# Kernel optimization log

Hardware: AMD Instinct MI355X
Metric: run time of the kernel (lower is better)

Reference implementation:

```python
import jax, jax.numpy as jnp
import numpy as np

B, T, H = 32, 4096, 512


def setup_inputs() -> dict:
    key = jax.random.key(0)
    k1, k2, k3, k4, k5 = jax.random.split(key, 5)
    stdv = 1.0 / np.sqrt(2 * H)
    stdv_v = 1.0 / np.sqrt(H)
    return {
        "hidden": jax.random.normal(k1, (B, H), dtype=jnp.float32),
        "encoder_outputs": jax.random.normal(k2, (T, B, H), dtype=jnp.float32),
        "W_attn": jax.random.uniform(k3, (H, 2 * H), minval=-stdv, maxval=stdv, dtype=jnp.float32),
        "b_attn": jax.random.uniform(k4, (H,), minval=-stdv, maxval=stdv, dtype=jnp.float32),
        "v": jax.random.uniform(k5, (H,), minval=-stdv_v, maxval=stdv_v, dtype=jnp.float32),
    }


def reference(hidden, encoder_outputs, W_attn, b_attn, v):
    # hidden: [B, H]; encoder_outputs: [T, B, H]
    T_ = encoder_outputs.shape[0]
    h = jnp.broadcast_to(hidden[None, :, :], (T_,) + hidden.shape).transpose(1, 0, 2)  # [B,T,H]
    enc = encoder_outputs.transpose(1, 0, 2)  # [B,T,H]
    cat = jnp.concatenate([h, enc], axis=2)  # [B,T,2H]
    # Linear(2H -> H) then legacy F.softmax with implicit dim=0 for 3D input (batch axis)
    energy = jax.nn.softmax(jnp.einsum('btk,hk->bth', cat, W_attn) + b_attn, axis=0)  # [B,T,H]
    # bmm(v[B,1,H], energy^T[B,H,T]) -> [B,1,T] -> squeeze -> [B,T]
    scores = jnp.einsum('h,bth->bt', v, energy)
    return jax.nn.relu(scores)[:, None, :]  # [B,1,T]
```

## Files before the change

kernel.cpp:

```cpp
#include <hip/hip_runtime.h>
#include <hip/hip_bf16.h>

#define B_ 32
#define T_ 4096
#define H_ 512
#define TILE_T 4
#define M_TILE 128
#define BK 64
#define KSTEPS 8
#define NTHREADS 512

typedef __attribute__((ext_vector_type(8))) short short8;
typedef __attribute__((ext_vector_type(8))) __bf16 bf16x8;
typedef __attribute__((ext_vector_type(4))) float f32x4;

__device__ __forceinline__ short f2bf(float f) {
    unsigned u = __builtin_bit_cast(unsigned, f);
    u = (u + 0x7fffu + ((u >> 16) & 1u)) >> 16;
    return (short)u;
}

__global__ void prep_w2(const float* __restrict__ W, short* __restrict__ w2p) {
    int idx = blockIdx.x * 256 + threadIdx.x;
    int kp = idx & 63;
    int h  = (idx >> 6) & 511;
    int s  = idx >> 15;
    int k  = kp ^ ((h & 7) << 3);
    w2p[idx] = f2bf(W[h * (2 * H_) + H_ + s * BK + k]);
}

__global__ void prep_hid(const float* __restrict__ hidden,
                         const float* __restrict__ W,
                         const float* __restrict__ bias,
                         float* __restrict__ hidproj) {
    __shared__ float hrow[H_];
    int b = blockIdx.y;
    int h = blockIdx.x * 128 + threadIdx.x;
    for (int i = threadIdx.x; i < H_; i += 128) hrow[i] = hidden[b * H_ + i];
    __syncthreads();
    const float* wr = W + (size_t)h * (2 * H_);
    float acc = bias[h];
#pragma unroll 4
    for (int k = 0; k < H_; k += 4) {
        acc += hrow[k]     * wr[k];
        acc += hrow[k + 1] * wr[k + 1];
        acc += hrow[k + 2] * wr[k + 2];
        acc += hrow[k + 3] * wr[k + 3];
    }
    hidproj[b * H_ + h] = acc;
}

__global__ __launch_bounds__(NTHREADS, 2)
void attn_main(const float* __restrict__ enc,
               const float* __restrict__ hidproj,
               const short* __restrict__ w2p,
               const float* __restrict__ vvec,
               float* __restrict__ out)
{
    __shared__ __align__(16) short lds_a[M_TILE * BK];
    __shared__ __align__(16) short lds_w[H_ * BK];

    const int tid  = threadIdx.x;
    const int lane = tid & 63;
    const int wid  = tid >> 6;
    const int t0   = blockIdx.x * TILE_T;
    const int n0   = wid * 64;
    const int lo   = lane & 15;
    const int hi4  = lane >> 4;

    f32x4 acc[8][4];
#pragma unroll
    for (int i = 0; i < 8; ++i)
#pragma unroll
        for (int j = 0; j < 4; ++j) acc[i][j] = f32x4{0.f, 0.f, 0.f, 0.f};

    const int s0row = tid >> 3;
    const int s0ks  = tid & 7;
    const float* encbase = enc + (size_t)(t0 * B_) * H_;

    for (int kk = 0; kk < KSTEPS; ++kk) {
        const short* wsrc = w2p + (size_t)kk * (H_ * BK);
#pragma unroll
        for (int r = 0; r < 8; ++r) {
            __builtin_amdgcn_global_load_lds(
                (const __attribute__((address_space(1))) void*)(wsrc + (r * 512 + tid) * 8),
                (__attribute__((address_space(3))) void*)(lds_w + (r * 512 + wid * 64) * 8),
                16, 0, 0);
        }
#pragma unroll
        for (int si = 0; si < 2; ++si) {
            int row = s0row + si * 64;
            const float* src = encbase + (size_t)row * H_ + kk * BK + s0ks * 8;
            f32x4 x0 = *(const f32x4*)(src);
            f32x4 x1 = *(const f32x4*)(src + 4);
            short8 pk;
            pk[0] = f2bf(x0[0]); pk[1] = f2bf(x0[1]); pk[2] = f2bf(x0[2]); pk[3] = f2bf(x0[3]);
            pk[4] = f2bf(x1[0]); pk[5] = f2bf(x1[1]); pk[6] = f2bf(x1[2]); pk[7] = f2bf(x1[3]);
            int kp = (s0ks ^ (row & 7)) * 8;
            *(short8*)&lds_a[row * BK + kp] = pk;
        }
        __syncthreads();

#pragma unroll
        for (int ks = 0; ks < 2; ++ks) {
            bf16x8 bfrag[4];
            int kbase = ks * 32 + hi4 * 8;
#pragma unroll
            for (int ni = 0; ni < 4; ++ni) {
                int hrow = n0 + ni * 16 + lo;
                int kp = kbase ^ ((hrow & 7) << 3);
                bfrag[ni] = *(const bf16x8*)&lds_w[hrow * BK + kp];
            }
#pragma unroll
            for (int mi = 0; mi < 8; ++mi) {
                int arow = mi * 16 + lo;
                int kp = kbase ^ ((arow & 7) << 3);
                bf16x8 afrag = *(const bf16x8*)&lds_a[arow * BK + kp];
#pragma unroll
                for (int ni = 0; ni < 4; ++ni)
                    acc[mi][ni] = __builtin_amdgcn_mfma_f32_16x16x32_bf16(
                        afrag, bfrag[ni], acc[mi][ni], 0, 0, 0);
            }
        }
        __syncthreads();
    }

    {
        float hp[2][4][4];
#pragma unroll
        for (int par = 0; par < 2; ++par)
#pragma unroll
            for (int j = 0; j < 4; ++j) {
                int b = par * 16 + hi4 * 4 + j;
#pragma unroll
                for (int ni = 0; ni < 4; ++ni)
                    hp[par][j][ni] = hidproj[b * H_ + n0 + ni * 16 + lo];
            }
#pragma unroll
        for (int mi = 0; mi < 8; ++mi)
#pragma unroll
            for (int ni = 0; ni < 4; ++ni)
#pragma unroll
                for (int j = 0; j < 4; ++j)
                    acc[mi][ni][j] += hp[mi & 1][j][ni];
    }

    float vh[4];
#pragma unroll
    for (int ni = 0; ni < 4; ++ni) vh[ni] = vvec[n0 + ni * 16 + lo];

    float scp[8][4];
#pragma unroll
    for (int tl = 0; tl < 4; ++tl) {
        const int m0 = tl * 2, m1 = tl * 2 + 1;
#pragma unroll
        for (int ni = 0; ni < 4; ++ni) {
            float mx = -1e30f;
#pragma unroll
            for (int j = 0; j < 4; ++j) {
                mx = fmaxf(mx, acc[m0][ni][j]);
                mx = fmaxf(mx, acc[m1][ni][j]);
            }
            mx = fmaxf(mx, __shfl_xor(mx, 16));
            mx = fmaxf(mx, __shfl_xor(mx, 32));
            float e0[4], e1[4];
            float sum = 0.f;
#pragma unroll
            for (int j = 0; j < 4; ++j) {
                e0[j] = __expf(acc[m0][ni][j] - mx);
                e1[j] = __expf(acc[m1][ni][j] - mx);
                sum += e0[j] + e1[j];
            }
            sum += __shfl_xor(sum, 16);
            sum += __shfl_xor(sum, 32);
            float rs = vh[ni] / sum;
#pragma unroll
            for (int j = 0; j < 4; ++j) {
                if (ni == 0) { scp[m0][j] = e0[j] * rs; scp[m1][j] = e1[j] * rs; }
                else         { scp[m0][j] += e0[j] * rs; scp[m1][j] += e1[j] * rs; }
            }
        }
    }

#pragma unroll
    for (int mi = 0; mi < 8; ++mi)
#pragma unroll
        for (int j = 0; j < 4; ++j) {
            float x = scp[mi][j];
            x += __shfl_xor(x, 1);
            x += __shfl_xor(x, 2);
            x += __shfl_xor(x, 4);
            x += __shfl_xor(x, 8);
            scp[mi][j] = x;
        }

    float* red = (float*)lds_a;
    if (lo == 0) {
#pragma unroll
        for (int mi = 0; mi < 8; ++mi)
#pragma unroll
            for (int j = 0; j < 4; ++j)
                red[wid * 128 + mi * 16 + hi4 * 4 + j] = scp[mi][j];
    }
    __syncthreads();
    if (tid < 128) {
        float s = 0.f;
#pragma unroll
        for (int w = 0; w < 8; ++w) s += red[w * 128 + tid];
        int b  = tid & 31;
        int tl = tid >> 5;
        out[(size_t)b * T_ + (t0 + tl)] = fmaxf(s, 0.f);
    }
}

extern "C" void kernel_launch(void* const* d_in, const int* in_sizes, int n_in,
                              void* d_out, int out_size, void* d_ws, size_t ws_size,
                              hipStream_t stream) {
    const float* hidden = (const float*)d_in[0];
    const float* enc    = (const float*)d_in[1];
    const float* W      = (const float*)d_in[2];
    const float* bias   = (const float*)d_in[3];
    const float* v      = (const float*)d_in[4];
    float* out = (float*)d_out;

    float* hidproj = (float*)d_ws;
    short* w2p     = (short*)((char*)d_ws + 65536);

    prep_w2<<<1024, 256, 0, stream>>>(W, w2p);
    prep_hid<<<dim3(4, 32), 128, 0, stream>>>(hidden, W, bias, hidproj);
    attn_main<<<T_ / TILE_T, NTHREADS, 0, stream>>>(enc, hidproj, w2p, v, out);
}
```

Before: 144.4 us.

## Load W fragments directly to registers and double-buffer encoder tiles in LDS

Pre-packs the bf16 weight into per-wave MFMA fragment order so each wave loads its B fragments straight from global/L2 into registers instead of staging all of W through LDS. Encoder tiles are double-buffered in LDS with BK raised to 128, so the next chunk is prefetched while MFMAs run and each K step needs one barrier instead of two. It also uses the packed v_cvt_pk_bf16_f32 instruction for conversion and s_setprio around MFMA bursts. This trades LDS traffic and capacity for more global/L2 reads of W per block and higher register pressure.

Result: slower. 232.9 us (+61.3%).

```diff
diff --git a/kernel.cpp b/kernel.cpp
--- a/kernel.cpp
+++ b/kernel.cpp
@@ -6,8 +6,8 @@
 #define H_ 512
 #define TILE_T 4
 #define M_TILE 128
-#define BK 64
-#define KSTEPS 8
+#define BK 128
+#define KSTEPS 4
 #define NTHREADS 512
 
 typedef __attribute__((ext_vector_type(8))) short short8;
@@ -20,13 +20,25 @@
     return (short)u;
 }
 
-__global__ void prep_w2(const float* __restrict__ W, short* __restrict__ w2p) {
+__device__ __forceinline__ short8 pack8(f32x4 a, f32x4 b) {
+    union { unsigned u[4]; short8 s; } r;
+    asm("v_cvt_pk_bf16_f32 %0, %1, %2" : "=v"(r.u[0]) : "v"(a[0]), "v"(a[1]));
+    asm("v_cvt_pk_bf16_f32 %0, %1, %2" : "=v"(r.u[1]) : "v"(a[2]), "v"(a[3]));
+    asm("v_cvt_pk_bf16_f32 %0, %1, %2" : "=v"(r.u[2]) : "v"(b[0]), "v"(b[1]));
+    asm("v_cvt_pk_bf16_f32 %0, %1, %2" : "=v"(r.u[3]) : "v"(b[2]), "v"(b[3]));
+    return r.s;
+}
+
+__global__ void prep_w2f(const float* __restrict__ W, short* __restrict__ w2f) {
     int idx = blockIdx.x * 256 + threadIdx.x;
-    int kp = idx & 63;
-    int h  = (idx >> 6) & 511;
-    int s  = idx >> 15;
-    int k  = kp ^ ((h & 7) << 3);
-    w2p[idx] = f2bf(W[h * (2 * H_) + H_ + s * BK + k]);
+    int j    = idx & 7;
+    int lane = (idx >> 3) & 63;
+    int ni   = (idx >> 9) & 3;
+    int ck   = (idx >> 11) & 15;
+    int c    = (idx >> 15) & 7;
+    int h = c * 64 + ni * 16 + (lane & 15);
+    int k = ck * 32 + (lane >> 4) * 8 + j;
+    w2f[idx] = f2bf(W[h * (2 * H_) + H_ + k]);
 }
 
 __global__ void prep_hid(const float* __restrict__ hidden,
@@ -53,12 +65,11 @@
 __global__ __launch_bounds__(NTHREADS, 2)
 void attn_main(const float* __restrict__ enc,
                const float* __restrict__ hidproj,
-               const short* __restrict__ w2p,
+               const short* __restrict__ w2f,
                const float* __restrict__ vvec,
                float* __restrict__ out)
 {
-    __shared__ __align__(16) short lds_a[M_TILE * BK];
-    __shared__ __align__(16) short lds_w[H_ * BK];
+    __shared__ __align__(16) short lds_a[2][M_TILE * BK];
 
     const int tid  = threadIdx.x;
     const int lane = tid & 63;
@@ -74,56 +85,104 @@
 #pragma unroll
         for (int j = 0; j < 4; ++j) acc[i][j] = f32x4{0.f, 0.f, 0.f, 0.f};
 
-    const int s0row = tid >> 3;
-    const int s0ks  = tid & 7;
-    const float* encbase = enc + (size_t)(t0 * B_) * H_;
-
+    const short* wbase = w2f + (size_t)wid * 32768 + lane * 8;
+
+    const int arow = tid >> 2;
+    const int akc  = tid & 3;
+    const float* abase = enc + (size_t)(t0 * B_ + arow) * H_ + akc * 32;
+    const int aw0 = arow * BK + (((akc * 4 + 0) ^ (arow & 7)) << 3);
+    const int aw1 = arow * BK + (((akc * 4 + 1) ^ (arow & 7)) << 3);
+    const int aw2 = arow * BK + (((akc * 4 + 2) ^ (arow & 7)) << 3);
+    const int aw3 = arow * BK + (((akc * 4 + 3) ^ (arow & 7)) << 3);
+
+    {
+        f32x4 y0 = *(const f32x4*)(abase);      f32x4 y1 = *(const f32x4*)(abase + 4);
+        f32x4 y2 = *(const f32x4*)(abase + 8);  f32x4 y3 = *(const f32x4*)(abase + 12);
+        f32x4 y4 = *(const f32x4*)(abase + 16); f32x4 y5 = *(const f32x4*)(abase + 20);
+        f32x4 y6 = *(const f32x4*)(abase + 24); f32x4 y7 = *(const f32x4*)(abase + 28);
+        *(short8*)&lds_a[0][aw0] = pack8(y0, y1);
+        *(short8*)&lds_a[0][aw1] = pack8(y2, y3);
+        *(short8*)&lds_a[0][aw2] = pack8(y4, y5);
+        *(short8*)&lds_a[0][aw3] = pack8(y6, y7);
+        asm volatile("s_waitcnt lgkmcnt(0)" ::: "memory");
+        __builtin_amdgcn_s_barrier();
+    }
+
+#define KSUB(S, BQ)                                                               \
+    {                                                                             \
+        bf16x8 af[4];                                                             \
+        _Pragma("unroll")                                                         \
+        for (int mi = 0; mi < 4; ++mi) {                                          \
+            int r = mi * 16 + lo;                                                 \
+            af[mi] = *(const bf16x8*)&ab[r * BK + ((((S) * 4 + hi4) ^ (r & 7)) << 3)]; \
+        }                                                                         \
+        __builtin_amdgcn_s_setprio(1);                                            \
+        _Pragma("unroll")                                                         \
+        for (int mi = 0; mi < 4; ++mi)                                            \
+            _Pragma("unroll")                                                     \
+            for (int ni = 0; ni < 4; ++ni)                                        \
+                acc[mi][ni] = __builtin_amdgcn_mfma_f32_16x16x32_bf16(            \
+                    af[mi], BQ[ni], acc[mi][ni], 0, 0, 0);                        \
+        __builtin_amdgcn_s_setprio(0);                                            \
+        _Pragma("unroll")                                                         \
+        for (int mi = 0; mi < 4; ++mi) {                                          \
+            int r = (mi + 4) * 16 + lo;                                           \
+            af[mi] = *(const bf16x8*)&ab[r * BK + ((((S) * 4 + hi4) ^ (r & 7)) << 3)]; \
+        }                                                                         \
+        __builtin_amdgcn_s_setprio(1);                                            \
+        _Pragma("unroll")                                                         \
+        for (int mi = 0; mi < 4; ++mi)                                            \
+            _Pragma("unroll")                                                     \
+            for (int ni = 0; ni < 4; ++ni)                                        \
+                acc[mi + 4][ni] = __builtin_amdgcn_mfma_f32_16x16x32_bf16(        \
+                    af[mi], BQ[ni], acc[mi + 4][ni], 0, 0, 0);                    \
+        __builtin_amdgcn_s_setprio(0);                                            \
+    }
+
+#pragma unroll 1
     for (int kk = 0; kk < KSTEPS; ++kk) {
-        const short* wsrc = w2p + (size_t)kk * (H_ * BK);
-#pragma unroll
-        for (int r = 0; r < 8; ++r) {
-            __builtin_amdgcn_global_load_lds(
-                (const __attribute__((address_space(1))) void*)(wsrc + (r * 512 + tid) * 8),
-                (__attribute__((address_space(3))) void*)(lds_w + (r * 512 + wid * 64) * 8),
-                16, 0, 0);
-        }
-#pragma unroll
-        for (int si = 0; si < 2; ++si) {
-            int row = s0row + si * 64;
-            const float* src = encbase + (size_t)row * H_ + kk * BK + s0ks * 8;
-            f32x4 x0 = *(const f32x4*)(src);
-            f32x4 x1 = *(const f32x4*)(src + 4);
-            short8 pk;
-            pk[0] = f2bf(x0[0]); pk[1] = f2bf(x0[1]); pk[2] = f2bf(x0[2]); pk[3] = f2bf(x0[3]);
-            pk[4] = f2bf(x1[0]); pk[5] = f2bf(x1[1]); pk[6] = f2bf(x1[2]); pk[7] = f2bf(x1[3]);
-            int kp = (s0ks ^ (row & 7)) * 8;
-            *(short8*)&lds_a[row * BK + kp] = pk;
-        }
-        __syncthreads();
-
-#pragma unroll
-        for (int ks = 0; ks < 2; ++ks) {
-            bf16x8 bfrag[4];
-            int kbase = ks * 32 + hi4 * 8;
-#pragma unroll
-            for (int ni = 0; ni < 4; ++ni) {
-                int hrow = n0 + ni * 16 + lo;
-                int kp = kbase ^ ((hrow & 7) << 3);
-                bfrag[ni] = *(const bf16x8*)&lds_w[hrow * BK + kp];
-            }
-#pragma unroll
-            for (int mi = 0; mi < 8; ++mi) {
-                int arow = mi * 16 + lo;
-                int kp = kbase ^ ((arow & 7) << 3);
-                bf16x8 afrag = *(const bf16x8*)&lds_a[arow * BK + kp];
-#pragma unroll
-                for (int ni = 0; ni < 4; ++ni)
-                    acc[mi][ni] = __builtin_amdgcn_mfma_f32_16x16x32_bf16(
-                        afrag, bfrag[ni], acc[mi][ni], 0, 0, 0);
-            }
-        }
-        __syncthreads();
-    }
+        const int cur = kk & 1;
+        const bool pf = (kk + 1) < KSTEPS;
+        const short* __restrict__ ab = &lds_a[cur][0];
+        short* __restrict__ adst = &lds_a[cur ^ 1][0];
+
+        f32x4 x0, x1, x2, x3, x4, x5, x6, x7;
+        if (pf) {
+            const float* asrc = abase + (size_t)(kk + 1) * BK;
+            x0 = *(const f32x4*)(asrc);      x1 = *(const f32x4*)(asrc + 4);
+            x2 = *(const f32x4*)(asrc + 8);  x3 = *(const f32x4*)(asrc + 12);
+            x4 = *(const f32x4*)(asrc + 16); x5 = *(const f32x4*)(asrc + 20);
+            x6 = *(const f32x4*)(asrc + 24); x7 = *(const f32x4*)(asrc + 28);
+        }
+
+        const int ck0 = kk * 4;
+        bf16x8 bqA[4], bqB[4];
+#pragma unroll
+        for (int ni = 0; ni < 4; ++ni) bqA[ni] = *(const bf16x8*)(wbase + ((ck0 + 0) * 4 + ni) * 512);
+#pragma unroll
+        for (int ni = 0; ni < 4; ++ni) bqB[ni] = *(const bf16x8*)(wbase + ((ck0 + 1) * 4 + ni) * 512);
+
+        KSUB(0, bqA)
+#pragma unroll
+        for (int ni = 0; ni < 4; ++ni) bqA[ni] = *(const bf16x8*)(wbase + ((ck0 + 2) * 4 + ni) * 512);
+        KSUB(1, bqB)
+#pragma unroll
+        for (int ni = 0; ni < 4; ++ni) bqB[ni] = *(const bf16x8*)(wbase + ((ck0 + 3) * 4 + ni) * 512);
+
+        if (pf) {
+            *(short8*)&adst[aw0] = pack8(x0, x1);
+            *(short8*)&adst[aw1] = pack8(x2, x3);
+            *(short8*)&adst[aw2] = pack8(x4, x5);
+            *(short8*)&adst[aw3] = pack8(x6, x7);
+        }
+
+        KSUB(2, bqA)
+        KSUB(3, bqB)
+
+        asm volatile("s_waitcnt lgkmcnt(0)" ::: "memory");
+        __builtin_amdgcn_s_barrier();
+    }
+#undef KSUB
 
     {
         float hp[2][4][4];
@@ -194,7 +253,8 @@
             scp[mi][j] = x;
         }
 
-    float* red = (float*)lds_a;
+    __syncthreads();
+    float* red = (float*)&lds_a[0][0];
     if (lo == 0) {
 #pragma unroll
         for (int mi = 0; mi < 8; ++mi)
@@ -224,9 +284,9 @@
     float* out = (float*)d_out;
 
     float* hidproj = (float*)d_ws;
-    short* w2p     = (short*)((char*)d_ws + 65536);
-
-    prep_w2<<<1024, 256, 0, stream>>>(W, w2p);
+    short* w2f     = (short*)((char*)d_ws + 65536);
+
+    prep_w2f<<<1024, 256, 0, stream>>>(W, w2f);
     prep_hid<<<dim3(4, 32), 128, 0, stream>>>(hidden, W, bias, hidproj);
-    attn_main<<<T_ / TILE_T, NTHREADS, 0, stream>>>(enc, hidproj, w2p, v, out);
-}
+    attn_main<<<T_ / TILE_T, NTHREADS, 0, stream>>>(enc, hidproj, w2f, v, out);
+}
```
